# Performance work log

Hardware: AMD Instinct MI355X
Metric: run time of the kernel (lower is better)

Reference implementation:

```python
import jax, jax.numpy as jnp
import numpy as np

V, E, H = 50257, 256, 128          # vocab, embedding_size, lstm hidden per direction
L, B = 2048, 64                    # seq_len, batch (x is [L, B], seq-first)
SEP, MASK = 50256, 0
SEP_EVERY = 16
N_UTT = L // SEP_EVERY             # utterances per sequence (seps planted regularly)


def setup_inputs() -> dict:
    key = jax.random.key(0)
    ks = jax.random.split(key, 12)
    x = jax.random.randint(ks[0], (L, B), 0, SEP, dtype=jnp.int32)
    # plant sep tokens every SEP_EVERY positions -> each utterance has SEP_EVERY tokens
    x = x.at[SEP_EVERY - 1::SEP_EVERY, :].set(SEP)
    s = 1.0 / np.sqrt(H)
    u = lambda k, sh: jax.random.uniform(k, sh, jnp.float32, -s, s)
    return {
        "x": x,
        "emb": jax.random.normal(ks[1], (V, E), jnp.float32),
        "w_ih_f": u(ks[2], (4 * H, E)), "w_hh_f": u(ks[3], (4 * H, H)),
        "b_ih_f": u(ks[4], (4 * H,)),   "b_hh_f": u(ks[5], (4 * H,)),
        "w_ih_b": u(ks[6], (4 * H, E)), "w_hh_b": u(ks[7], (4 * H, H)),
        "b_ih_b": u(ks[8], (4 * H,)),   "b_hh_b": u(ks[9], (4 * H,)),
        "w_out": u(ks[10], (2, E)),     "b_out": u(ks[11], (2,)),
    }


def _lstm_dir(xu, w_ih, w_hh, b_ih, b_hh, reverse):
    # xu: [T, B, E]; PyTorch LSTM gate order i, f, g, o
    xp = jnp.einsum("tbe,ge->tbg", xu, w_ih) + b_ih + b_hh  # [T, B, 4H]

    def step(carry, xt):
        h, c = carry
        g = xt + h @ w_hh.T
        i, f, gg, o = jnp.split(g, 4, axis=-1)
        c = jax.nn.sigmoid(f) * c + jax.nn.sigmoid(i) * jnp.tanh(gg)
        h = jax.nn.sigmoid(o) * jnp.tanh(c)
        return (h, c), h

    init = (jnp.zeros((xu.shape[1], H), xu.dtype), jnp.zeros((xu.shape[1], H), xu.dtype))
    _, hs = jax.lax.scan(step, init, xp, reverse=reverse)
    return hs  # [T, B, H]


def _forward(x, emb, w_ih_f, w_hh_f, b_ih_f, b_hh_f, w_ih_b, w_hh_b, b_ih_b, b_hh_b, w_out, b_out):
    # --- ragged utterance mean-pool (replaces per-token Python loops) ---
    seps = (x == SEP)
    seg = jnp.cumsum(seps.astype(jnp.int32), axis=0) - seps.astype(jnp.int32)  # [L,B]: utterance id per token (sep ends its utterance)
    gids = (seg * B + jnp.arange(B, dtype=jnp.int32)[None, :]).reshape(L * B)
    tok_emb = emb[x]                                              # [L, B, E]
    sums = jax.ops.segment_sum(tok_emb.reshape(L * B, E), gids, num_segments=N_UTT * B).reshape(N_UTT, B, E)
    cnts = jax.ops.segment_sum(jnp.ones((L * B,), tok_emb.dtype), gids, num_segments=N_UTT * B).reshape(N_UTT, B, 1)
    u = jnp.where(cnts > 0, sums / jnp.maximum(cnts, 1.0), 0.0)   # [N_UTT, B, E] (zeros pad, as original)
    # --- BiLSTM over utterances ---
    h_f = _lstm_dir(u, w_ih_f, w_hh_f, b_ih_f, b_hh_f, reverse=False)
    h_b = _lstm_dir(u, w_ih_b, w_hh_b, b_ih_b, b_hh_b, reverse=True)
    h = jnp.concatenate([h_f, h_b], axis=-1)                      # [N_UTT, B, E]
    logits = jnp.einsum("tbe,oe->tbo", h, w_out) + b_out          # [N_UTT, B, 2]
    policy = jax.nn.softmax(logits, axis=-1)
    # greedy policy (deterministic reference)
    u_mask = jnp.argmax(policy, axis=-1)                          # [N_UTT, B] in {0,1}
    chosen_policy = jnp.take_along_axis(policy, u_mask[..., None], axis=-1)  # [N_UTT, B, 1]
    # expand utterance mask to token mask and mask the input
    token_mask = u_mask.astype(bool)[seg, jnp.arange(B)[None, :]]  # [L, B]
    masked_input = jnp.where(token_mask, x, MASK)
    return logits, policy, chosen_policy, u_mask.astype(bool), masked_input


def reference(x, emb, w_ih_f, w_hh_f, b_ih_f, b_hh_f, w_ih_b, w_hh_b, b_ih_b, b_hh_b, w_out, b_out):
    return _forward(x, emb, w_ih_f, w_hh_f, b_ih_f, b_hh_f, w_ih_b, w_hh_b, b_ih_b, b_hh_b, w_out, b_out)
```

## Files before the change

kernel.cpp:

```cpp
#include <hip/hip_runtime.h>
#include <math.h>

#define LL   2048
#define BB   64
#define EE   256
#define HH   128
#define GG   512
#define TT   128
#define SEPT 50256

__global__ __launch_bounds__(256) void segscan_k(
    const int* __restrict__ x, int* __restrict__ seg,
    int* __restrict__ cnt, int* __restrict__ start)
{
    int b   = blockIdx.x;
    int tid = threadIdx.x;
    __shared__ int tsum[256];
    __shared__ int ucnt[TT];
    __shared__ int ustart[TT];

    int flags[8];
    int local = 0;
#pragma unroll
    for (int i = 0; i < 8; i++) {
        int t = tid * 8 + i;
        flags[i] = (x[t * BB + b] == SEPT) ? 1 : 0;
        local += flags[i];
    }
    tsum[tid] = local;
    __syncthreads();
    int val = local;
    for (int off = 1; off < 256; off <<= 1) {
        int other = (tid >= off) ? tsum[tid - off] : 0;
        __syncthreads();
        val += other;
        tsum[tid] = val;
        __syncthreads();
    }
    int excl = val - local;

    if (tid < TT) ucnt[tid] = 0;
    __syncthreads();
    int run = excl;
#pragma unroll
    for (int i = 0; i < 8; i++) {
        int t = tid * 8 + i;
        int s = run;
        seg[t * BB + b] = s;
        run += flags[i];
        if (s < TT) atomicAdd(&ucnt[s], 1);
    }
    __syncthreads();
    if (tid == 0) {
        int acc = 0;
        for (int u = 0; u < TT; u++) { ustart[u] = acc; acc += ucnt[u]; }
    }
    __syncthreads();
    if (tid < TT) {
        cnt[tid * BB + b]   = ucnt[tid];
        start[tid * BB + b] = ustart[tid];
    }
}

__global__ __launch_bounds__(256) void pool_k(
    const int* __restrict__ x, const float* __restrict__ emb,
    const int* __restrict__ cnt, const int* __restrict__ start,
    float* __restrict__ up)
{
    int wid  = threadIdx.x >> 6;
    int lane = threadIdx.x & 63;
    int bid  = blockIdx.x * 4 + wid;
    int b    = bid & 63;
    int c    = cnt[bid];
    int st   = start[bid];

    float4 acc = {0.f, 0.f, 0.f, 0.f};
    int tok = (c > 0) ? x[st * BB + b] : 0;
    for (int j = 0; j < c; j++) {
        int tok_n = (j + 1 < c) ? x[(st + j + 1) * BB + b] : 0;
        float4 v = ((const float4*)(emb + (size_t)tok * EE))[lane];
        acc.x += v.x; acc.y += v.y; acc.z += v.z; acc.w += v.w;
        tok = tok_n;
    }
    float inv = (c > 0) ? 1.f / (float)c : 0.f;
    float4 r = {acc.x * inv, acc.y * inv, acc.z * inv, acc.w * inv};
    ((float4*)(up + (size_t)bid * EE))[lane] = r;
}

__global__ __launch_bounds__(256) void xp_gemm_k(
    const float* __restrict__ A,
    const float* __restrict__ wf, const float* __restrict__ wb,
    const float* __restrict__ bihf, const float* __restrict__ bhhf,
    const float* __restrict__ bihb, const float* __restrict__ bhhb,
    float* __restrict__ C)
{
    __shared__ float As[32][128];
    __shared__ float Bs[32][128];
    int tid  = threadIdx.x;
    int row0 = blockIdx.x * 128;
    int col0 = blockIdx.y * 128;
    int tx = tid & 15, ty = tid >> 4;
    float acc[8][8] = {};

    for (int k0 = 0; k0 < EE; k0 += 32) {
#pragma unroll
        for (int i = 0; i < 4; i++) {
            int idx = tid + i * 256;
            int m   = idx >> 3;
            int k4  = idx & 7;
            float4 av = *(const float4*)(A + (size_t)(row0 + m) * EE + k0 + k4 * 4);
            As[k4 * 4 + 0][m] = av.x; As[k4 * 4 + 1][m] = av.y;
            As[k4 * 4 + 2][m] = av.z; As[k4 * 4 + 3][m] = av.w;
        }
#pragma unroll
        for (int i = 0; i < 4; i++) {
            int idx = tid + i * 256;
            int n   = idx >> 3;
            int k4  = idx & 7;
            int gc  = col0 + n;
            const float* wsrc = (gc < GG) ? (wf + (size_t)gc * EE)
                                          : (wb + (size_t)(gc - GG) * EE);
            float4 bv = *(const float4*)(wsrc + k0 + k4 * 4);
            Bs[k4 * 4 + 0][n] = bv.x; Bs[k4 * 4 + 1][n] = bv.y;
            Bs[k4 * 4 + 2][n] = bv.z; Bs[k4 * 4 + 3][n] = bv.w;
        }
        __syncthreads();
#pragma unroll
        for (int k = 0; k < 32; k++) {
            float a8[8], b8[8];
            *(float4*)&a8[0] = *(const float4*)&As[k][ty * 8 + 0];
            *(float4*)&a8[4] = *(const float4*)&As[k][ty * 8 + 4];
            *(float4*)&b8[0] = *(const float4*)&Bs[k][tx * 8 + 0];
            *(float4*)&b8[4] = *(const float4*)&Bs[k][tx * 8 + 4];
#pragma unroll
            for (int i = 0; i < 8; i++)
#pragma unroll
                for (int j = 0; j < 8; j++)
                    acc[i][j] += a8[i] * b8[j];
        }
        __syncthreads();
    }

    float bias[8];
#pragma unroll
    for (int j = 0; j < 8; j++) {
        int gc = col0 + tx * 8 + j;
        bias[j] = (gc < GG) ? (bihf[gc] + bhhf[gc])
                            : (bihb[gc - GG] + bhhb[gc - GG]);
    }
#pragma unroll
    for (int i = 0; i < 8; i++) {
        int r = row0 + ty * 8 + i;
        float4 v0 = {acc[i][0] + bias[0], acc[i][1] + bias[1],
                     acc[i][2] + bias[2], acc[i][3] + bias[3]};
        float4 v1 = {acc[i][4] + bias[4], acc[i][5] + bias[5],
                     acc[i][6] + bias[6], acc[i][7] + bias[7]};
        *(float4*)(C + (size_t)r * 1024 + col0 + tx * 8 + 0) = v0;
        *(float4*)(C + (size_t)r * 1024 + col0 + tx * 8 + 4) = v1;
    }
}

__device__ __forceinline__ float sigm_f(float x) {
    return 1.f / (1.f + __expf(-x));
}
__device__ __forceinline__ float tanh_f(float x) {
    return 1.f - 2.f / (__expf(2.f * x) + 1.f);
}

__global__ __launch_bounds__(512) void lstm_rec_k(
    const float* __restrict__ xp,
    const float* __restrict__ whh_f, const float* __restrict__ whh_b,
    float* __restrict__ hout)
{
    int bid = blockIdx.x;
    int dir = bid >> 6;
    int b   = bid & 63;
    int tid = threadIdx.x;
    int wv  = tid >> 6;
    int l   = tid & 63;
    const float* whh = dir ? whh_b : whh_f;

    float4 w4[32];
#pragma unroll
    for (int j = 0; j < 8; j++) {
        const float* src = whh + (size_t)(l + 64 * j) * HH + 16 * wv;
#pragma unroll
        for (int k4 = 0; k4 < 4; k4++) {
            asm volatile("global_load_dwordx4 %0, %1, off"
                         : "=v"(w4[j * 4 + k4])
                         : "v"(src + k4 * 4)
                         : "memory");
        }
    }
    asm volatile("s_waitcnt vmcnt(0)" ::: "memory");
    __builtin_amdgcn_sched_barrier(0);

    __shared__ __align__(16) float h_lds[HH];
    __shared__ float part[GG][9];
    __shared__ float act[GG];

    int g    = tid;
    int sect = g >> 7;

    float c = 0.f;
    if (g < HH) h_lds[g] = 0.f;
    __syncthreads();

    int t0   = dir ? (TT - 1) : 0;
    float xg = xp[(size_t)(t0 * BB + b) * 1024 + dir * GG + g];

    for (int s = 0; s < TT; s++) {
        float hs[16];
#pragma unroll
        for (int k4 = 0; k4 < 4; k4++)
            *(float4*)&hs[k4 * 4] = *(const float4*)&h_lds[wv * 16 + k4 * 4];

        float acc[8] = {0.f, 0.f, 0.f, 0.f, 0.f, 0.f, 0.f, 0.f};
#pragma unroll
        for (int k = 0; k < 16; k++) {
            float hk = hs[k];
#pragma unroll
            for (int j = 0; j < 8; j++) {
                const float4 q = w4[j * 4 + (k >> 2)];
                float wjk = ((k & 3) == 0) ? q.x
                          : ((k & 3) == 1) ? q.y
                          : ((k & 3) == 2) ? q.z : q.w;
                acc[j] += wjk * hk;
            }
        }

        float xg_next = xg;
        if (s < TT - 1) {
            int tn = dir ? (TT - 2 - s) : (s + 1);
            xg_next = xp[(size_t)(tn * BB + b) * 1024 + dir * GG + g];
        }

#pragma unroll
        for (int j = 0; j < 8; j++)
            part[l + 64 * j][wv] = acc[j];
        __syncthreads();

        float sum = xg;
#pragma unroll
        for (int w2 = 0; w2 < 8; w2++)
            sum += part[g][w2];
        act[g] = (sect == 2) ? tanh_f(sum) : sigm_f(sum);
        __syncthreads();

        if (tid < HH) {
            float si = act[tid], sf = act[HH + tid];
            float tg = act[2 * HH + tid], so = act[3 * HH + tid];
            c = sf * c + si * tg;
            float h = so * tanh_f(c);
            h_lds[tid] = h;
            int t = dir ? (TT - 1 - s) : s;
            hout[((size_t)(dir * TT + t) * BB + b) * HH + tid] = h;
        }
        xg = xg_next;
        __syncthreads();
    }
}

__global__ __launch_bounds__(256) void head_k(
    const float* __restrict__ hbuf,
    const float* __restrict__ wout, const float* __restrict__ bout,
    float* __restrict__ out)
{
    int wid  = threadIdx.x >> 6;
    int lane = threadIdx.x & 63;
    int row  = blockIdx.x * 4 + wid;
    int t = row >> 6, b = row & 63;
    const float* hf = hbuf + ((size_t)(t)      * BB + b) * HH;
    const float* hb = hbuf + ((size_t)(TT + t) * BB + b) * HH;

    float l0 = 0.f, l1 = 0.f, v;
    v = hf[lane];      l0 += v * wout[lane];           l1 += v * wout[256 + lane];
    v = hf[lane + 64]; l0 += v * wout[64 + lane];      l1 += v * wout[320 + lane];
    v = hb[lane];      l0 += v * wout[128 + lane];     l1 += v * wout[384 + lane];
    v = hb[lane + 64]; l0 += v * wout[192 + lane];     l1 += v * wout[448 + lane];
#pragma unroll
    for (int off = 32; off > 0; off >>= 1) {
        l0 += __shfl_down(l0, off);
        l1 += __shfl_down(l1, off);
    }
    if (lane == 0) {
        l0 += bout[0]; l1 += bout[1];
        float m  = fmaxf(l0, l1);
        float e0 = __expf(l0 - m), e1 = __expf(l1 - m);
        float inv = 1.f / (e0 + e1);
        float p0 = e0 * inv, p1 = e1 * inv;
        int amax = (l1 > l0) ? 1 : 0;
        out[(size_t)row * 2 + 0] = l0;
        out[(size_t)row * 2 + 1] = l1;
        out[16384 + (size_t)row * 2 + 0] = p0;
        out[16384 + (size_t)row * 2 + 1] = p1;
        out[32768 + row] = amax ? p1 : p0;
        out[40960 + row] = (float)amax;
    }
}

__global__ __launch_bounds__(256) void mask_k(
    const int* __restrict__ x, const int* __restrict__ seg,
    const float* __restrict__ umask, float* __restrict__ out4)
{
    int idx = blockIdx.x * 256 + threadIdx.x;
    int b = idx & 63;
    int s = seg[idx];
    if (s > TT - 1) s = TT - 1;
    if (s < 0) s = 0;
    float keep = umask[s * BB + b];
    out4[idx] = (keep != 0.f) ? (float)x[idx] : 0.f;
}

extern "C" void kernel_launch(void* const* d_in, const int* in_sizes, int n_in,
                              void* d_out, int out_size, void* d_ws, size_t ws_size,
                              hipStream_t stream)
{
    const int*   x    = (const int*)  d_in[0];
    const float* emb  = (const float*)d_in[1];
    const float* wihf = (const float*)d_in[2];
    const float* whhf = (const float*)d_in[3];
    const float* bihf = (const float*)d_in[4];
    const float* bhhf = (const float*)d_in[5];
    const float* wihb = (const float*)d_in[6];
    const float* whhb = (const float*)d_in[7];
    const float* bihb = (const float*)d_in[8];
    const float* bhhb = (const float*)d_in[9];
    const float* wout = (const float*)d_in[10];
    const float* bout = (const float*)d_in[11];
    float* out = (float*)d_out;
    char*  ws  = (char*)d_ws;

    int*   seg   = (int*)  (ws + 0);
    int*   cnt   = (int*)  (ws + 524288);
    int*   start = (int*)  (ws + 557056);
    float* up    = (float*)(ws + 589824);
    float* xp    = (float*)(ws + 8978432);
    float* hbuf  = (float*)(ws + 42532864);

    segscan_k<<<64, 256, 0, stream>>>(x, seg, cnt, start);
    pool_k<<<2048, 256, 0, stream>>>(x, emb, cnt, start, up);
    xp_gemm_k<<<dim3(64, 8), 256, 0, stream>>>(up, wihf, wihb, bihf, bhhf, bihb, bhhb, xp);
    lstm_rec_k<<<128, 512, 0, stream>>>(xp, whhf, whhb, hbuf);
    head_k<<<2048, 256, 0, stream>>>(hbuf, wout, bout, out);
    mask_k<<<512, 256, 0, stream>>>(x, seg, out + 40960, out + 49152);
}
```

Baseline: 297.5 us.

## Restructure LSTM recurrence to 1024 threads with two-way K split per gate

The recurrent kernel now runs 1024 threads per block. Each thread owns one gate row and half of the hidden dimension (64 weights held in registers), so the reduction across 8 waves through a padded LDS array becomes a two-way partial sum. The separate activation pass and its extra barrier are removed: 128 threads sum both partials, apply all four gate nonlinearities and update the cell directly, which saves one __syncthreads per step. In exchange the xp prefetch is now done only by those 128 threads after the state update, and these serial global loads may land on the critical path. The larger block also puts more register pressure on each wave.

```diff
diff --git a/kernel.cpp b/kernel.cpp
--- a/kernel.cpp
+++ b/kernel.cpp
@@ -167,7 +167,7 @@
     return 1.f - 2.f / (__expf(2.f * x) + 1.f);
 }
 
-__global__ __launch_bounds__(512) void lstm_rec_k(
+__global__ __launch_bounds__(1024) void lstm_rec_k(
     const float* __restrict__ xp,
     const float* __restrict__ whh_f, const float* __restrict__ whh_b,
     float* __restrict__ hout)
@@ -176,87 +176,76 @@
     int dir = bid >> 6;
     int b   = bid & 63;
     int tid = threadIdx.x;
-    int wv  = tid >> 6;
-    int l   = tid & 63;
+    int g   = tid & 511;
+    int kap = tid >> 9;
     const float* whh = dir ? whh_b : whh_f;
 
-    float4 w4[32];
-#pragma unroll
-    for (int j = 0; j < 8; j++) {
-        const float* src = whh + (size_t)(l + 64 * j) * HH + 16 * wv;
-#pragma unroll
-        for (int k4 = 0; k4 < 4; k4++) {
+    float4 wr[16];
+    {
+        const float* wbase = whh + (size_t)g * HH + 64 * kap;
+#pragma unroll
+        for (int q = 0; q < 16; q++) {
             asm volatile("global_load_dwordx4 %0, %1, off"
-                         : "=v"(w4[j * 4 + k4])
-                         : "v"(src + k4 * 4)
-                         : "memory");
+                         : "=v"(wr[q]) : "v"(wbase + q * 4) : "memory");
         }
     }
     asm volatile("s_waitcnt vmcnt(0)" ::: "memory");
     __builtin_amdgcn_sched_barrier(0);
 
     __shared__ __align__(16) float h_lds[HH];
-    __shared__ float part[GG][9];
-    __shared__ float act[GG];
-
-    int g    = tid;
-    int sect = g >> 7;
+    __shared__ float part[2][GG];
 
     float c = 0.f;
-    if (g < HH) h_lds[g] = 0.f;
-    __syncthreads();
-
-    int t0   = dir ? (TT - 1) : 0;
-    float xg = xp[(size_t)(t0 * BB + b) * 1024 + dir * GG + g];
+    if (tid < HH) h_lds[tid] = 0.f;
+    __syncthreads();
+
+    int t0 = dir ? (TT - 1) : 0;
+    float xg4[4];
+    if (tid < HH) {
+        const float* xrow = xp + (size_t)(t0 * BB + b) * 1024 + dir * GG;
+        xg4[0] = xrow[tid];
+        xg4[1] = xrow[HH + tid];
+        xg4[2] = xrow[2 * HH + tid];
+        xg4[3] = xrow[3 * HH + tid];
+    }
 
     for (int s = 0; s < TT; s++) {
-        float hs[16];
-#pragma unroll
-        for (int k4 = 0; k4 < 4; k4++)
-            *(float4*)&hs[k4 * 4] = *(const float4*)&h_lds[wv * 16 + k4 * 4];
-
-        float acc[8] = {0.f, 0.f, 0.f, 0.f, 0.f, 0.f, 0.f, 0.f};
-#pragma unroll
-        for (int k = 0; k < 16; k++) {
-            float hk = hs[k];
-#pragma unroll
-            for (int j = 0; j < 8; j++) {
-                const float4 q = w4[j * 4 + (k >> 2)];
-                float wjk = ((k & 3) == 0) ? q.x
-                          : ((k & 3) == 1) ? q.y
-                          : ((k & 3) == 2) ? q.z : q.w;
-                acc[j] += wjk * hk;
-            }
-        }
-
-        float xg_next = xg;
-        if (s < TT - 1) {
-            int tn = dir ? (TT - 2 - s) : (s + 1);
-            xg_next = xp[(size_t)(tn * BB + b) * 1024 + dir * GG + g];
-        }
-
-#pragma unroll
-        for (int j = 0; j < 8; j++)
-            part[l + 64 * j][wv] = acc[j];
-        __syncthreads();
-
-        float sum = xg;
-#pragma unroll
-        for (int w2 = 0; w2 < 8; w2++)
-            sum += part[g][w2];
-        act[g] = (sect == 2) ? tanh_f(sum) : sigm_f(sum);
+        float pacc = 0.f;
+#pragma unroll
+        for (int q = 0; q < 16; q++) {
+            float4 hv = *(const float4*)&h_lds[64 * kap + q * 4];
+            float4 wq = wr[q];
+            pacc += wq.x * hv.x;
+            pacc += wq.y * hv.y;
+            pacc += wq.z * hv.z;
+            pacc += wq.w * hv.w;
+        }
+        part[kap][g] = pacc;
         __syncthreads();
 
         if (tid < HH) {
-            float si = act[tid], sf = act[HH + tid];
-            float tg = act[2 * HH + tid], so = act[3 * HH + tid];
+            int i = tid;
+            float s_i = xg4[0] + part[0][i]            + part[1][i];
+            float s_f = xg4[1] + part[0][HH + i]       + part[1][HH + i];
+            float s_g = xg4[2] + part[0][2 * HH + i]   + part[1][2 * HH + i];
+            float s_o = xg4[3] + part[0][3 * HH + i]   + part[1][3 * HH + i];
+            float si = sigm_f(s_i), sf = sigm_f(s_f);
+            float tg = tanh_f(s_g), so = sigm_f(s_o);
             c = sf * c + si * tg;
             float h = so * tanh_f(c);
-            h_lds[tid] = h;
+            h_lds[i] = h;
             int t = dir ? (TT - 1 - s) : s;
-            hout[((size_t)(dir * TT + t) * BB + b) * HH + tid] = h;
-        }
-        xg = xg_next;
+            hout[((size_t)(dir * TT + t) * BB + b) * HH + i] = h;
+
+            if (s < TT - 1) {
+                int tn = dir ? (TT - 2 - s) : (s + 1);
+                const float* xrow = xp + (size_t)(tn * BB + b) * 1024 + dir * GG;
+                xg4[0] = xrow[i];
+                xg4[1] = xrow[HH + i];
+                xg4[2] = xrow[2 * HH + i];
+                xg4[3] = xrow[3 * HH + i];
+            }
+        }
         __syncthreads();
     }
 }
@@ -341,7 +330,7 @@
     segscan_k<<<64, 256, 0, stream>>>(x, seg, cnt, start);
     pool_k<<<2048, 256, 0, stream>>>(x, emb, cnt, start, up);
     xp_gemm_k<<<dim3(64, 8), 256, 0, stream>>>(up, wihf, wihb, bihf, bhhf, bihb, bhhb, xp);
-    lstm_rec_k<<<128, 512, 0, stream>>>(xp, whhf, whhb, hbuf);
+    lstm_rec_k<<<128, 1024, 0, stream>>>(xp, whhf, whhb, hbuf);
     head_k<<<2048, 256, 0, stream>>>(hbuf, wout, bout, out);
     mask_k<<<512, 256, 0, stream>>>(x, seg, out + 40960, out + 49152);
 }
```

New measurement: 313.9 us. 1.06x slower.

## Split LSTM recurrent matvec across 1024 threads with half the gate rows each

Applied to the files above, without the earlier changes.

The recurrent kernel now launches 1024 threads per block instead of 512. Each wave holds weights for 4 gate-row groups instead of 8, and the work is split over 8 k-slices and 2 row halves. This halves the per-thread register weight footprint and the serial FMA chain on each timestep's critical path. The cost is more waves contending at each __syncthreads, and half the threads sit idle during the gate activation and reduction phases.

```diff
diff --git a/kernel.cpp b/kernel.cpp
--- a/kernel.cpp
+++ b/kernel.cpp
@@ -167,7 +167,7 @@
     return 1.f - 2.f / (__expf(2.f * x) + 1.f);
 }
 
-__global__ __launch_bounds__(512) void lstm_rec_k(
+__global__ __launch_bounds__(1024, 4) void lstm_rec_k(
     const float* __restrict__ xp,
     const float* __restrict__ whh_f, const float* __restrict__ whh_b,
     float* __restrict__ hout)
@@ -178,19 +178,22 @@
     int tid = threadIdx.x;
     int wv  = tid >> 6;
     int l   = tid & 63;
+    int kap = wv & 7;
+    int jh  = (wv >> 3) * 4;
     const float* whh = dir ? whh_b : whh_f;
 
-    float4 w4[32];
-#pragma unroll
-    for (int j = 0; j < 8; j++) {
-        const float* src = whh + (size_t)(l + 64 * j) * HH + 16 * wv;
-#pragma unroll
-        for (int k4 = 0; k4 < 4; k4++) {
-            asm volatile("global_load_dwordx4 %0, %1, off"
-                         : "=v"(w4[j * 4 + k4])
-                         : "v"(src + k4 * 4)
-                         : "memory");
-        }
+    float4 w4[16];
+#pragma unroll
+    for (int jj = 0; jj < 4; jj++) {
+        const float* src = whh + (size_t)(l + 64 * (jh + jj)) * HH + 16 * kap;
+        asm volatile("global_load_dwordx4 %0, %1, off"
+                     : "=v"(w4[jj * 4 + 0]) : "v"(src) : "memory");
+        asm volatile("global_load_dwordx4 %0, %1, off offset:16"
+                     : "=v"(w4[jj * 4 + 1]) : "v"(src) : "memory");
+        asm volatile("global_load_dwordx4 %0, %1, off offset:32"
+                     : "=v"(w4[jj * 4 + 2]) : "v"(src) : "memory");
+        asm volatile("global_load_dwordx4 %0, %1, off offset:48"
+                     : "=v"(w4[jj * 4 + 3]) : "v"(src) : "memory");
     }
     asm volatile("s_waitcnt vmcnt(0)" ::: "memory");
     __builtin_amdgcn_sched_barrier(0);
@@ -200,51 +203,54 @@
     __shared__ float act[GG];
 
     int g    = tid;
-    int sect = g >> 7;
+    int sect = (g >> 7) & 3;
 
     float c = 0.f;
-    if (g < HH) h_lds[g] = 0.f;
+    if (tid < HH) h_lds[tid] = 0.f;
     __syncthreads();
 
     int t0   = dir ? (TT - 1) : 0;
-    float xg = xp[(size_t)(t0 * BB + b) * 1024 + dir * GG + g];
+    float xg = 0.f;
+    if (tid < GG)
+        xg = xp[(size_t)(t0 * BB + b) * 1024 + dir * GG + g];
 
     for (int s = 0; s < TT; s++) {
         float hs[16];
 #pragma unroll
-        for (int k4 = 0; k4 < 4; k4++)
-            *(float4*)&hs[k4 * 4] = *(const float4*)&h_lds[wv * 16 + k4 * 4];
-
-        float acc[8] = {0.f, 0.f, 0.f, 0.f, 0.f, 0.f, 0.f, 0.f};
-#pragma unroll
-        for (int k = 0; k < 16; k++) {
-            float hk = hs[k];
-#pragma unroll
-            for (int j = 0; j < 8; j++) {
-                const float4 q = w4[j * 4 + (k >> 2)];
-                float wjk = ((k & 3) == 0) ? q.x
-                          : ((k & 3) == 1) ? q.y
-                          : ((k & 3) == 2) ? q.z : q.w;
-                acc[j] += wjk * hk;
+        for (int q = 0; q < 4; q++)
+            *(float4*)&hs[q * 4] = *(const float4*)&h_lds[16 * kap + q * 4];
+
+        float acc[4] = {0.f, 0.f, 0.f, 0.f};
+#pragma unroll
+        for (int jj = 0; jj < 4; jj++) {
+#pragma unroll
+            for (int q = 0; q < 4; q++) {
+                float4 wq = w4[jj * 4 + q];
+                acc[jj] += wq.x * hs[q * 4 + 0];
+                acc[jj] += wq.y * hs[q * 4 + 1];
+                acc[jj] += wq.z * hs[q * 4 + 2];
+                acc[jj] += wq.w * hs[q * 4 + 3];
             }
         }
 
         float xg_next = xg;
-        if (s < TT - 1) {
+        if (tid < GG && s < TT - 1) {
             int tn = dir ? (TT - 2 - s) : (s + 1);
             xg_next = xp[(size_t)(tn * BB + b) * 1024 + dir * GG + g];
         }
 
 #pragma unroll
-        for (int j = 0; j < 8; j++)
-            part[l + 64 * j][wv] = acc[j];
-        __syncthreads();
-
-        float sum = xg;
-#pragma unroll
-        for (int w2 = 0; w2 < 8; w2++)
-            sum += part[g][w2];
-        act[g] = (sect == 2) ? tanh_f(sum) : sigm_f(sum);
+        for (int jj = 0; jj < 4; jj++)
+            part[l + 64 * (jh + jj)][kap] = acc[jj];
+        __syncthreads();
+
+        if (tid < GG) {
+            float sum = xg;
+#pragma unroll
+            for (int w2 = 0; w2 < 8; w2++)
+                sum += part[g][w2];
+            act[g] = (sect == 2) ? tanh_f(sum) : sigm_f(sum);
+        }
         __syncthreads();
 
         if (tid < HH) {
@@ -341,7 +347,7 @@
     segscan_k<<<64, 256, 0, stream>>>(x, seg, cnt, start);
     pool_k<<<2048, 256, 0, stream>>>(x, emb, cnt, start, up);
     xp_gemm_k<<<dim3(64, 8), 256, 0, stream>>>(up, wihf, wihb, bihf, bhhf, bihb, bhhb, xp);
-    lstm_rec_k<<<128, 512, 0, stream>>>(xp, whhf, whhb, hbuf);
+    lstm_rec_k<<<128, 1024, 0, stream>>>(xp, whhf, whhb, hbuf);
     head_k<<<2048, 256, 0, stream>>>(hbuf, wout, bout, out);
     mask_k<<<512, 256, 0, stream>>>(x, seg, out + 40960, out + 49152);
 }
```

Result: no change. 301.1 us (+1.2%).
